# Kernel optimization log

Measured on AMD Instinct MI355X. Metric: run time of the kernel, lower is better.

The kernel has to match this reference:

```python
import jax, jax.numpy as jnp
import numpy as np

D = 1024
H = 16
HD = D // H
B = 4
N = 2048


def setup_inputs() -> dict:
    key = jax.random.key(0)
    ks = jax.random.split(key, 5)
    x = jax.random.normal(ks[0], (B, N, D), dtype=jnp.float32)
    # nn.Linear(D, 3D): weight [3D, D], bias [3D]; y = x @ W.T + b
    w_qkv = jax.random.normal(ks[1], (3 * D, D), dtype=jnp.float32) * (1.0 / np.sqrt(D))
    b_qkv = jax.random.normal(ks[2], (3 * D,), dtype=jnp.float32) * 0.02
    w_out = jax.random.normal(ks[3], (D, D), dtype=jnp.float32) * (1.0 / np.sqrt(D))
    b_out = jax.random.normal(ks[4], (D,), dtype=jnp.float32) * 0.02
    return {"x": x, "w_qkv": w_qkv, "b_qkv": b_qkv, "w_out": w_out, "b_out": b_out}


def reference(x, w_qkv, b_qkv, w_out, b_out):
    Bn, Nn, Dn = x.shape
    scale = HD ** (-0.5)
    qkv = x @ w_qkv.T + b_qkv                      # [B, N, 3D]
    q, k, v = jnp.split(qkv, 3, axis=-1)
    # [B, N, D] -> [B, H, N, HD]
    def heads(t):
        return t.reshape(Bn, Nn, H, HD).transpose(0, 2, 1, 3)
    q, k, v = heads(q), heads(k), heads(v)
    scores = jnp.einsum('bhqd,bhkd->bhqk', q, k) * scale   # [B, H, N, N]
    causal = jnp.tril(jnp.ones((Nn, Nn), dtype=bool))
    scores = jnp.where(causal[None, None], scores, jnp.float32(-jnp.inf))
    alpha = jax.nn.softmax(scores, axis=-1)
    out = jnp.einsum('bhqk,bhkd->bhqd', alpha, v)          # [B, H, N, HD]
    out = out.transpose(0, 2, 1, 3).reshape(Bn, Nn, Dn)
    return out @ w_out.T + b_out
```

## Files before the change

kernel.cpp:

```cpp
#include <hip/hip_runtime.h>
#include <hip/hip_bf16.h>

#define D_MODEL 1024
#define H_HEADS 16
#define HD 64
#define B_BATCH 4
#define N_SEQ 2048
#define BH (B_BATCH*H_HEADS)
#define M_TOT (B_BATCH*N_SEQ)
#define N_QKV (3*D_MODEL)
#define QSCALE 0.18033688011112042f

typedef __bf16 bf16x8 __attribute__((ext_vector_type(8)));
typedef __bf16 bf16x4 __attribute__((ext_vector_type(4)));
typedef float f32x4 __attribute__((ext_vector_type(4)));

__device__ inline ushort cvt_bf16(float f){
  return __builtin_bit_cast(ushort, (__bf16)f);
}

#define GLOAD_LDS16(g, l) __builtin_amdgcn_global_load_lds( \
    (const __attribute__((address_space(1))) void*)(g), \
    (__attribute__((address_space(3))) void*)(l), 16, 0, 0)

__global__ void cvt_f32_bf16_kernel(const float* __restrict__ src, ushort* __restrict__ dst, int n){
  int i = (blockIdx.x*blockDim.x + threadIdx.x)*4;
  int stride = gridDim.x*blockDim.x*4;
  for (; i < n; i += stride){
    float4 f = *reinterpret_cast<const float4*>(src+i);
    ushort4 u;
    u.x=cvt_bf16(f.x); u.y=cvt_bf16(f.y); u.z=cvt_bf16(f.z); u.w=cvt_bf16(f.w);
    *reinterpret_cast<ushort4*>(dst+i) = u;
  }
}

template<int MODE>
__global__ __launch_bounds__(256) void gemm_bt(
    const ushort* __restrict__ A, const ushort* __restrict__ Wt,
    const float* __restrict__ bias, void* __restrict__ out,
    int M, int Ncols, int K)
{
  constexpr int BM=128, BN=128, BK=32;
  __shared__ __align__(16) ushort As[BM][BK];
  __shared__ __align__(16) ushort Bs[BN][BK];
  const int tid = threadIdx.x;
  const int w = tid>>6, lane = tid&63;
  const int wm = w>>1, wn = w&1;
  const int row0 = blockIdx.y*BM, col0 = blockIdx.x*BN;
  const int lr = lane&15, lko = (lane>>4)*8;
  f32x4 acc[4][4] = {};

  for (int k0=0; k0<K; k0+=BK) {
    __syncthreads();
    #pragma unroll
    for (int i=0;i<2;i++){
      int rbase = (i*4+w)*16;
      int r = rbase + (lane>>2);
      int c = (lane&3)*8;
      GLOAD_LDS16(&A [(size_t)(row0+r)*K + k0 + c], &As[rbase][0]);
      GLOAD_LDS16(&Wt[(size_t)(col0+r)*K + k0 + c], &Bs[rbase][0]);
    }
    __syncthreads();
    bf16x8 af[4], bfr[4];
    #pragma unroll
    for (int m=0;m<4;m++)
      af[m] = *reinterpret_cast<const bf16x8*>(&As[wm*64 + m*16 + lr][lko]);
    #pragma unroll
    for (int n=0;n<4;n++)
      bfr[n] = *reinterpret_cast<const bf16x8*>(&Bs[wn*64 + n*16 + lr][lko]);
    #pragma unroll
    for (int m=0;m<4;m++)
      #pragma unroll
      for (int n=0;n<4;n++)
        acc[m][n] = __builtin_amdgcn_mfma_f32_16x16x32_bf16(af[m], bfr[n], acc[m][n], 0,0,0);
  }

  const int orow_base = row0 + wm*64;
  const int ocol_base = col0 + wn*64;
  #pragma unroll
  for (int m=0;m<4;m++){
    #pragma unroll
    for(int n=0;n<4;n++){
      const int gc = ocol_base + n*16 + (lane&15);
      const float bv = bias[gc];
      const int gr0 = orow_base + m*16 + (lane>>4)*4;
      float vals[4];
      #pragma unroll
      for (int r=0;r<4;r++) vals[r] = acc[m][n][r] + bv;
      if (MODE==0){
        const int which = gc >> 10;
        const int d = gc & 1023;
        const int h = d >> 6, hd = d & 63;
        const int b = gr0 >> 11, nn0 = gr0 & 2047;
        ushort* o = (ushort*)out;
        if (which==2){
          ushort4 u;
          u.x=cvt_bf16(vals[0]); u.y=cvt_bf16(vals[1]);
          u.z=cvt_bf16(vals[2]); u.w=cvt_bf16(vals[3]);
          *reinterpret_cast<ushort4*>(
            &o[2ull*BH*N_SEQ*HD + ((size_t)(b*H_HEADS+h)*HD + hd)*N_SEQ + nn0]) = u;
        } else {
          const float sc = (which==0) ? QSCALE : 1.0f;
          #pragma unroll
          for (int r=0;r<4;r++)
            o[(size_t)which*((size_t)BH*N_SEQ*HD)
              + ((size_t)(b*H_HEADS+h)*N_SEQ + nn0 + r)*HD + hd] = cvt_bf16(vals[r]*sc);
        }
      } else {
        #pragma unroll
        for (int r=0;r<4;r++)
          ((float*)out)[(size_t)(gr0+r)*Ncols + gc] = vals[r];
      }
    }
  }
}

__global__ __launch_bounds__(256,3) void attn_mfma(
    const ushort* __restrict__ q, const ushort* __restrict__ kg, const ushort* __restrict__ vtg,
    ushort* __restrict__ attn_out)
{
  __shared__ __align__(16) ushort Ks[2][64][64];
  __shared__ __align__(16) ushort Vs[2][64][64];
  __shared__ __align__(16) ushort Ps[4][32][72];
  const int tid=threadIdx.x, w=tid>>6, lane=tid&63;
  const int lr=lane&15, lk=lane>>4;
  const int bid = blockIdx.x;
  const int strip = 15 - (bid>>6);
  const int bh = bid & 63;
  const size_t base=(size_t)bh*N_SEQ*HD;
  const ushort* kb = kg + base;
  const ushort* vb = vtg + base;
  const int b = bh>>4, h = bh&15;

  const int s_roff = lane>>3;
  const int s_g    = (lane&7) ^ s_roff;
  int rd_base[2];
  #pragma unroll
  for (int ks=0;ks<2;ks++)
    rd_base[ks] = lr*64 + (((ks*4+lk) ^ (lr&7))*8);

  const int row0 = strip*128;
  const int wrow = row0 + w*32;
  const int nt = 2*strip + 2;

  bf16x8 qf[2][2];
  #pragma unroll
  for (int qt=0;qt<2;qt++)
    #pragma unroll
    for (int ks=0;ks<2;ks++)
      qf[qt][ks] = *reinterpret_cast<const bf16x8*>(
          &q[base + (size_t)(wrow + qt*16 + lr)*HD + ks*32 + lk*8]);

  f32x4 o_acc[2][4] = {};
  float mrun[2] = {-1e30f,-1e30f}, lrun[2] = {0.f,0.f};

  {
    const int r0k = w*16, rA = r0k + s_roff;
    GLOAD_LDS16(&kb[(size_t)(rA)*HD + s_g*8],       &Ks[0][r0k][0]);
    GLOAD_LDS16(&kb[(size_t)(rA+8)*HD + s_g*8],     &Ks[0][r0k+8][0]);
    GLOAD_LDS16(&vb[(size_t)(rA)*N_SEQ + s_g*8],    &Vs[0][r0k][0]);
    GLOAD_LDS16(&vb[(size_t)(rA+8)*N_SEQ + s_g*8],  &Vs[0][r0k+8][0]);
  }
  int cur = 0;
  for (int t=0;t<nt;t++){
    __syncthreads();
    if (t+1 < nt){
      const int j1 = (t+1)*64;
      const int r0k = w*16, rA = r0k + s_roff;
      GLOAD_LDS16(&kb[(size_t)(j1+rA)*HD + s_g*8],        &Ks[cur^1][r0k][0]);
      GLOAD_LDS16(&kb[(size_t)(j1+rA+8)*HD + s_g*8],      &Ks[cur^1][r0k+8][0]);
      GLOAD_LDS16(&vb[(size_t)(rA)*N_SEQ + j1 + s_g*8],   &Vs[cur^1][r0k][0]);
      GLOAD_LDS16(&vb[(size_t)(rA+8)*N_SEQ + j1 + s_g*8], &Vs[cur^1][r0k+8][0]);
    }
    const int j0 = t*64;
    if (j0 <= wrow + 31){
      const ushort* Kt = &Ks[cur][0][0];
      const ushort* Vt = &Vs[cur][0][0];
      f32x4 sacc[2][4] = {};
      __builtin_amdgcn_s_setprio(1);
      #pragma unroll
      for (int ks=0;ks<2;ks++)
        #pragma unroll
        for (int kt=0;kt<4;kt++){
          bf16x8 kf = *reinterpret_cast<const bf16x8*>(Kt + kt*1024 + rd_base[ks]);
          sacc[0][kt] = __builtin_amdgcn_mfma_f32_16x16x32_bf16(kf, qf[0][ks], sacc[0][kt], 0,0,0);
          sacc[1][kt] = __builtin_amdgcn_mfma_f32_16x16x32_bf16(kf, qf[1][ks], sacc[1][kt], 0,0,0);
        }
      __builtin_amdgcn_s_setprio(0);

      const bool tailmask = (j0 + 63 > wrow);
      #pragma unroll
      for (int qt=0;qt<2;qt++){
        const int qrow = wrow + qt*16 + lr;
        if (tailmask){
          #pragma unroll
          for (int kt=0;kt<4;kt++)
            #pragma unroll
            for (int r=0;r<4;r++)
              if (j0 + kt*16 + lk*4 + r > qrow) sacc[qt][kt][r] = -1e30f;
        }
        float mx = -1e30f;
        #pragma unroll
        for (int kt=0;kt<4;kt++)
          #pragma unroll
          for (int r=0;r<4;r++) mx = fmaxf(mx, sacc[qt][kt][r]);
        mx = fmaxf(mx, __shfl_xor(mx, 16));
        mx = fmaxf(mx, __shfl_xor(mx, 32));
        float mcur = mrun[qt];
        if (__any(mx - mcur > 8.0f)){
          const float mnew = fmaxf(mcur, mx);
          const float corr = exp2f(mcur - mnew);
          mrun[qt] = mnew; mcur = mnew;
          lrun[qt] *= corr;
          #pragma unroll
          for (int dt=0;dt<4;dt++) o_acc[qt][dt] *= corr;
        }
        float sum = 0.f;
        #pragma unroll
        for (int kt=0;kt<4;kt++){
          float p0 = exp2f(sacc[qt][kt][0]-mcur);
          float p1 = exp2f(sacc[qt][kt][1]-mcur);
          float p2 = exp2f(sacc[qt][kt][2]-mcur);
          float p3 = exp2f(sacc[qt][kt][3]-mcur);
          sum += (p0+p1)+(p2+p3);
          bf16x4 pk;
          pk[0]=(__bf16)p0; pk[1]=(__bf16)p1; pk[2]=(__bf16)p2; pk[3]=(__bf16)p3;
          *reinterpret_cast<bf16x4*>(&Ps[w][qt*16+lr][kt*16+lk*4]) = pk;
        }
        lrun[qt] += sum;
      }

      #pragma unroll
      for (int ks=0;ks<2;ks++){
        bf16x8 pa0 = *reinterpret_cast<const bf16x8*>(&Ps[w][lr][ks*32+lk*8]);
        bf16x8 pa1 = *reinterpret_cast<const bf16x8*>(&Ps[w][16+lr][ks*32+lk*8]);
        __builtin_amdgcn_s_setprio(1);
        #pragma unroll
        for (int dt=0;dt<4;dt++){
          bf16x8 vf = *reinterpret_cast<const bf16x8*>(Vt + dt*1024 + rd_base[ks]);
          o_acc[0][dt] = __builtin_amdgcn_mfma_f32_16x16x32_bf16(vf, pa0, o_acc[0][dt], 0,0,0);
          o_acc[1][dt] = __builtin_amdgcn_mfma_f32_16x16x32_bf16(vf, pa1, o_acc[1][dt], 0,0,0);
        }
        __builtin_amdgcn_s_setprio(0);
      }
    }
    cur ^= 1;
  }

  #pragma unroll
  for (int qt=0;qt<2;qt++){
    float rl = lrun[qt];
    rl += __shfl_xor(rl, 16);
    rl += __shfl_xor(rl, 32);
    const float rinv = 1.0f / rl;
    const size_t rowb = ((size_t)(b*N_SEQ) + wrow + qt*16 + lr)*D_MODEL + h*HD;
    #pragma unroll
    for (int dt=0;dt<4;dt++){
      bf16x4 u;
      u[0]=(__bf16)(o_acc[qt][dt][0]*rinv);
      u[1]=(__bf16)(o_acc[qt][dt][1]*rinv);
      u[2]=(__bf16)(o_acc[qt][dt][2]*rinv);
      u[3]=(__bf16)(o_acc[qt][dt][3]*rinv);
      *reinterpret_cast<bf16x4*>(&attn_out[rowb + dt*16 + lk*4]) = u;
    }
  }
}

extern "C" void kernel_launch(void* const* d_in, const int* in_sizes, int n_in,
                              void* d_out, int out_size, void* d_ws, size_t ws_size,
                              hipStream_t stream){
  const float* x     = (const float*)d_in[0];
  const float* w_qkv = (const float*)d_in[1];
  const float* b_qkv = (const float*)d_in[2];
  const float* w_out = (const float*)d_in[3];
  const float* b_out = (const float*)d_in[4];

  char* ws = (char*)d_ws;
  size_t off = 0;
  ushort* x_bf    = (ushort*)(ws+off); off += (size_t)M_TOT*D_MODEL*2;
  ushort* wqkv_bf = (ushort*)(ws+off); off += (size_t)N_QKV*D_MODEL*2;
  ushort* wout_bf = (ushort*)(ws+off); off += (size_t)D_MODEL*D_MODEL*2;
  ushort* qkv     = (ushort*)(ws+off); off += 3ull*BH*N_SEQ*HD*2;
  ushort* attn_o  = (ushort*)(ws+off); off += (size_t)M_TOT*D_MODEL*2;

  cvt_f32_bf16_kernel<<<1024, 256, 0, stream>>>(x,     x_bf,    M_TOT*D_MODEL);
  cvt_f32_bf16_kernel<<<512,  256, 0, stream>>>(w_qkv, wqkv_bf, N_QKV*D_MODEL);
  cvt_f32_bf16_kernel<<<256,  256, 0, stream>>>(w_out, wout_bf, D_MODEL*D_MODEL);

  dim3 g1(N_QKV/128, M_TOT/128);
  gemm_bt<0><<<g1, 256, 0, stream>>>(x_bf, wqkv_bf, b_qkv, qkv, M_TOT, N_QKV, D_MODEL);

  const ushort* qb  = qkv;
  const ushort* kb  = qkv + (size_t)BH*N_SEQ*HD;
  const ushort* vtb = qkv + 2ull*BH*N_SEQ*HD;
  attn_mfma<<<1024, 256, 0, stream>>>(qb, kb, vtb, attn_o);

  dim3 g3(D_MODEL/128, M_TOT/128);
  gemm_bt<2><<<g3, 256, 0, stream>>>(attn_o, wout_bf, b_out, (float*)d_out, M_TOT, D_MODEL, D_MODEL);
}
```

Baseline: 191.5 us.

## Replace GEMM with 8-wave double-buffered swizzled-LDS pipelined kernel

Replaces the 4-wave 128x128x32 GEMM with a 512-thread 128x256x64 kernel. It double-buffers LDS with an XOR-swizzled layout and splits each K-step into four MFMA phases, issuing global-to-LDS loads for the next tile between them. Explicit vmcnt/lgkmcnt waits, barriers and setprio are meant to overlap memory traffic with MFMA work and reduce LDS bank conflicts in both the QKV and output projections. The trade-off is many more barriers and a fragile hand-counted wait scheme, and the wider tile yields fewer blocks for the output GEMM.

```diff
diff --git a/kernel.cpp b/kernel.cpp
--- a/kernel.cpp
+++ b/kernel.cpp
@@ -15,6 +15,8 @@
 typedef __bf16 bf16x4 __attribute__((ext_vector_type(4)));
 typedef float f32x4 __attribute__((ext_vector_type(4)));
 
+#define MFMA16 __builtin_amdgcn_mfma_f32_16x16x32_bf16
+
 __device__ inline ushort cvt_bf16(float f){
   return __builtin_bit_cast(ushort, (__bf16)f);
 }
@@ -35,44 +37,116 @@
 }
 
 template<int MODE>
-__global__ __launch_bounds__(256) void gemm_bt(
+__global__ __launch_bounds__(512,2) void gemm8p(
     const ushort* __restrict__ A, const ushort* __restrict__ Wt,
     const float* __restrict__ bias, void* __restrict__ out,
     int M, int Ncols, int K)
 {
-  constexpr int BM=128, BN=128, BK=32;
-  __shared__ __align__(16) ushort As[BM][BK];
-  __shared__ __align__(16) ushort Bs[BN][BK];
+  constexpr int BM=128, BN=256, BK=64;
+  __shared__ __align__(16) ushort As[2][2][BM/2][64];
+  __shared__ __align__(16) ushort Bs[2][2][BN/2][64];
   const int tid = threadIdx.x;
   const int w = tid>>6, lane = tid&63;
-  const int wm = w>>1, wn = w&1;
+  const int wm = w>>2, wn = w&3;
   const int row0 = blockIdx.y*BM, col0 = blockIdx.x*BN;
-  const int lr = lane&15, lko = (lane>>4)*8;
+  const int lr = lane&15, lk = lane>>4;
+  const int s_r   = lane>>3;
+  const int c_log = (lane&7) ^ s_r;
+  const int g_dr  = (c_log>>2);
+  const int g_dc  = (c_log&3)*8;
+  const int rdc   = (((lr&1)*4 + lk) ^ ((lr>>1)&7)) * 8;
   f32x4 acc[4][4] = {};
 
-  for (int k0=0; k0<K; k0+=BK) {
-    __syncthreads();
-    #pragma unroll
-    for (int i=0;i<2;i++){
-      int rbase = (i*4+w)*16;
-      int r = rbase + (lane>>2);
-      int c = (lane&3)*8;
-      GLOAD_LDS16(&A [(size_t)(row0+r)*K + k0 + c], &As[rbase][0]);
-      GLOAD_LDS16(&Wt[(size_t)(col0+r)*K + k0 + c], &Bs[rbase][0]);
-    }
-    __syncthreads();
-    bf16x8 af[4], bfr[4];
+  auto stageA = [&](int buf, int kt, int ks){
+    GLOAD_LDS16(&A[(size_t)(row0 + 2*(w*8+s_r) + g_dr)*K + kt*BK + ks*32 + g_dc],
+                &As[buf][ks][w*8][0]);
+  };
+  auto stageB = [&](int buf, int kt, int ks, int u){
+    GLOAD_LDS16(&Wt[(size_t)(col0 + u*128 + 2*(w*8+s_r) + g_dr)*K + kt*BK + ks*32 + g_dc],
+                &Bs[buf][ks][u*64 + w*8][0]);
+  };
+
+  const int NT = K/BK;
+  stageA(0,0,0); stageB(0,0,0,0); stageB(0,0,0,1);
+  stageA(0,0,1); stageB(0,0,1,0); stageB(0,0,1,1);
+  asm volatile("s_waitcnt vmcnt(3)" ::: "memory");
+  __builtin_amdgcn_s_barrier();
+
+  int cur = 0;
+  for (int kt=0; kt<NT; ++kt){
+    const bool last = (kt == NT-1);
+    const int nb = cur^1;
+    bf16x8 af[4], bfr[2];
+
     #pragma unroll
     for (int m=0;m<4;m++)
-      af[m] = *reinterpret_cast<const bf16x8*>(&As[wm*64 + m*16 + lr][lko]);
-    #pragma unroll
-    for (int n=0;n<4;n++)
-      bfr[n] = *reinterpret_cast<const bf16x8*>(&Bs[wn*64 + n*16 + lr][lko]);
+      af[m] = *reinterpret_cast<const bf16x8*>(&As[cur][0][wm*32 + m*8 + (lr>>1)][rdc]);
+    bfr[0] = *reinterpret_cast<const bf16x8*>(&Bs[cur][0][wn*32 + 0  + (lr>>1)][rdc]);
+    bfr[1] = *reinterpret_cast<const bf16x8*>(&Bs[cur][0][wn*32 + 8  + (lr>>1)][rdc]);
+    if (!last){ stageA(nb, kt+1, 0); stageB(nb, kt+1, 0, 0); }
+    __builtin_amdgcn_s_barrier();
+    asm volatile("s_waitcnt lgkmcnt(0)" ::: "memory");
+    __builtin_amdgcn_sched_barrier(0);
+    __builtin_amdgcn_s_setprio(1);
+    #pragma unroll
+    for (int m=0;m<4;m++){
+      acc[m][0] = MFMA16(af[m], bfr[0], acc[m][0], 0,0,0);
+      acc[m][1] = MFMA16(af[m], bfr[1], acc[m][1], 0,0,0);
+    }
+    __builtin_amdgcn_s_setprio(0);
+    __builtin_amdgcn_s_barrier();
+
+    bfr[0] = *reinterpret_cast<const bf16x8*>(&Bs[cur][0][wn*32 + 16 + (lr>>1)][rdc]);
+    bfr[1] = *reinterpret_cast<const bf16x8*>(&Bs[cur][0][wn*32 + 24 + (lr>>1)][rdc]);
+    if (!last){ stageB(nb, kt+1, 0, 1); stageA(nb, kt+1, 1); }
+    __builtin_amdgcn_s_barrier();
+    asm volatile("s_waitcnt lgkmcnt(0)" ::: "memory");
+    __builtin_amdgcn_sched_barrier(0);
+    __builtin_amdgcn_s_setprio(1);
+    #pragma unroll
+    for (int m=0;m<4;m++){
+      acc[m][2] = MFMA16(af[m], bfr[0], acc[m][2], 0,0,0);
+      acc[m][3] = MFMA16(af[m], bfr[1], acc[m][3], 0,0,0);
+    }
+    __builtin_amdgcn_s_setprio(0);
+    if (last) asm volatile("s_waitcnt vmcnt(0)" ::: "memory");
+    else      asm volatile("s_waitcnt vmcnt(4)" ::: "memory");
+    __builtin_amdgcn_s_barrier();
+
     #pragma unroll
     for (int m=0;m<4;m++)
-      #pragma unroll
-      for (int n=0;n<4;n++)
-        acc[m][n] = __builtin_amdgcn_mfma_f32_16x16x32_bf16(af[m], bfr[n], acc[m][n], 0,0,0);
+      af[m] = *reinterpret_cast<const bf16x8*>(&As[cur][1][wm*32 + m*8 + (lr>>1)][rdc]);
+    bfr[0] = *reinterpret_cast<const bf16x8*>(&Bs[cur][1][wn*32 + 0  + (lr>>1)][rdc]);
+    bfr[1] = *reinterpret_cast<const bf16x8*>(&Bs[cur][1][wn*32 + 8  + (lr>>1)][rdc]);
+    if (!last) stageB(nb, kt+1, 1, 0);
+    __builtin_amdgcn_s_barrier();
+    asm volatile("s_waitcnt lgkmcnt(0)" ::: "memory");
+    __builtin_amdgcn_sched_barrier(0);
+    __builtin_amdgcn_s_setprio(1);
+    #pragma unroll
+    for (int m=0;m<4;m++){
+      acc[m][0] = MFMA16(af[m], bfr[0], acc[m][0], 0,0,0);
+      acc[m][1] = MFMA16(af[m], bfr[1], acc[m][1], 0,0,0);
+    }
+    __builtin_amdgcn_s_setprio(0);
+    __builtin_amdgcn_s_barrier();
+
+    bfr[0] = *reinterpret_cast<const bf16x8*>(&Bs[cur][1][wn*32 + 16 + (lr>>1)][rdc]);
+    bfr[1] = *reinterpret_cast<const bf16x8*>(&Bs[cur][1][wn*32 + 24 + (lr>>1)][rdc]);
+    if (!last) stageB(nb, kt+1, 1, 1);
+    __builtin_amdgcn_s_barrier();
+    asm volatile("s_waitcnt lgkmcnt(0)" ::: "memory");
+    __builtin_amdgcn_sched_barrier(0);
+    __builtin_amdgcn_s_setprio(1);
+    #pragma unroll
+    for (int m=0;m<4;m++){
+      acc[m][2] = MFMA16(af[m], bfr[0], acc[m][2], 0,0,0);
+      acc[m][3] = MFMA16(af[m], bfr[1], acc[m][3], 0,0,0);
+    }
+    __builtin_amdgcn_s_setprio(0);
+    if (!last) asm volatile("s_waitcnt vmcnt(3)" ::: "memory");
+    __builtin_amdgcn_s_barrier();
+    cur ^= 1;
   }
 
   const int orow_base = row0 + wm*64;
@@ -81,9 +155,9 @@
   for (int m=0;m<4;m++){
     #pragma unroll
     for(int n=0;n<4;n++){
-      const int gc = ocol_base + n*16 + (lane&15);
+      const int gc = ocol_base + n*16 + lr;
       const float bv = bias[gc];
-      const int gr0 = orow_base + m*16 + (lane>>4)*4;
+      const int gr0 = orow_base + m*16 + lk*4;
       float vals[4];
       #pragma unroll
       for (int r=0;r<4;r++) vals[r] = acc[m][n][r] + bv;
@@ -183,8 +257,8 @@
         #pragma unroll
         for (int kt=0;kt<4;kt++){
           bf16x8 kf = *reinterpret_cast<const bf16x8*>(Kt + kt*1024 + rd_base[ks]);
-          sacc[0][kt] = __builtin_amdgcn_mfma_f32_16x16x32_bf16(kf, qf[0][ks], sacc[0][kt], 0,0,0);
-          sacc[1][kt] = __builtin_amdgcn_mfma_f32_16x16x32_bf16(kf, qf[1][ks], sacc[1][kt], 0,0,0);
+          sacc[0][kt] = MFMA16(kf, qf[0][ks], sacc[0][kt], 0,0,0);
+          sacc[1][kt] = MFMA16(kf, qf[1][ks], sacc[1][kt], 0,0,0);
         }
       __builtin_amdgcn_s_setprio(0);
 
@@ -238,8 +312,8 @@
         #pragma unroll
         for (int dt=0;dt<4;dt++){
           bf16x8 vf = *reinterpret_cast<const bf16x8*>(Vt + dt*1024 + rd_base[ks]);
-          o_acc[0][dt] = __builtin_amdgcn_mfma_f32_16x16x32_bf16(vf, pa0, o_acc[0][dt], 0,0,0);
-          o_acc[1][dt] = __builtin_amdgcn_mfma_f32_16x16x32_bf16(vf, pa1, o_acc[1][dt], 0,0,0);
+          o_acc[0][dt] = MFMA16(vf, pa0, o_acc[0][dt], 0,0,0);
+          o_acc[1][dt] = MFMA16(vf, pa1, o_acc[1][dt], 0,0,0);
         }
         __builtin_amdgcn_s_setprio(0);
       }
@@ -287,14 +361,14 @@
   cvt_f32_bf16_kernel<<<512,  256, 0, stream>>>(w_qkv, wqkv_bf, N_QKV*D_MODEL);
   cvt_f32_bf16_kernel<<<256,  256, 0, stream>>>(w_out, wout_bf, D_MODEL*D_MODEL);
 
-  dim3 g1(N_QKV/128, M_TOT/128);
-  gemm_bt<0><<<g1, 256, 0, stream>>>(x_bf, wqkv_bf, b_qkv, qkv, M_TOT, N_QKV, D_MODEL);
+  dim3 g1(N_QKV/256, M_TOT/128);
+  gemm8p<0><<<g1, 512, 0, stream>>>(x_bf, wqkv_bf, b_qkv, qkv, M_TOT, N_QKV, D_MODEL);
 
   const ushort* qb  = qkv;
   const ushort* kb  = qkv + (size_t)BH*N_SEQ*HD;
   const ushort* vtb = qkv + 2ull*BH*N_SEQ*HD;
   attn_mfma<<<1024, 256, 0, stream>>>(qb, kb, vtb, attn_o);
 
-  dim3 g3(D_MODEL/128, M_TOT/128);
-  gemm_bt<2><<<g3, 256, 0, stream>>>(attn_o, wout_bf, b_out, (float*)d_out, M_TOT, D_MODEL, D_MODEL);
-}
+  dim3 g3(D_MODEL/256, M_TOT/128);
+  gemm8p<2><<<g3, 512, 0, stream>>>(attn_o, wout_bf, b_out, (float*)d_out, M_TOT, D_MODEL, D_MODEL);
+}
```

New measurement: 195.4 us. 2.0% more time.
